# Kernel tuning notes

Hardware: AMD Instinct MI355X
Metric: run time of the kernel (lower is better)

## Reference

```python
import math
import jax, jax.numpy as jnp
import numpy as np

N_HEADS = 16


def setup_inputs() -> dict:
    key = jax.random.key(0)
    k1, k2 = jax.random.split(key)
    qkv = jax.random.normal(k1, (2, 3072, 2048), dtype=jnp.float32)
    mask = jax.random.randint(k2, (2, 1, 2048), 0, 2).astype(jnp.bool_)
    return {"qkv": qkv, "mask": mask}


def reference(qkv, mask):
    bs, width, length = qkv.shape
    ch = width // (3 * N_HEADS)
    q, k, v = jnp.split(qkv, 3, axis=1)  # each [bs, H*C, T]
    scale = 1.0 / math.sqrt(math.sqrt(ch))  # applied to both q and k
    q = (q * scale).reshape(bs * N_HEADS, ch, length)
    k = (k * scale).reshape(bs * N_HEADS, ch, length)
    # [B*H, T, T] scores
    weight = jnp.einsum('bct,bcs->bts', q, k)
    # mask: [bs, 1, T] bool, True = valid token
    inv = ~mask[:, 0, :]                      # [bs, T]
    pad = inv[:, None, :] | inv[:, :, None]   # [bs, T, T]
    pad = jnp.broadcast_to(pad[:, None], (bs, N_HEADS, length, length))
    pad = pad.reshape(bs * N_HEADS, length, length)
    weight = jnp.where(pad, jnp.finfo(weight.dtype).min, weight)
    weight = jax.nn.softmax(weight.astype(jnp.float32), axis=-1).astype(qkv.dtype)
    a = jnp.einsum('bts,bcs->bct', weight, v.reshape(bs * N_HEADS, ch, length))
    return a.reshape(bs, N_HEADS * ch, length)
```

## Files before the change

kernel.cpp:

```cpp
#include <hip/hip_runtime.h>
#include <float.h>


typedef __attribute__((ext_vector_type(8))) short bf16x8;
typedef __attribute__((ext_vector_type(4))) float f32x4;
typedef __attribute__((ext_vector_type(16))) float f32x16;

#define TSEQ 2048
#define QT_OFF 0L
#define KF_OFF 4194304L
#define VF_OFF 8388608L

#if __has_builtin(__builtin_amdgcn_exp2f)
#define EXPFN(x) __builtin_amdgcn_exp2f(x)
#define SM_SCALE (0.125f * 1.44269504088896f)
#else
#define EXPFN(x) __expf(x)
#define SM_SCALE 0.125f
#endif

__device__ inline short f2bf(float x) {
    union { float f; unsigned u; } un; un.f = x;
    unsigned r = un.u + 0x7fffu + ((un.u >> 16) & 1u);
    return (short)(r >> 16);
}

__device__ inline unsigned cvtpk(float lo, float hi) {
    unsigned r;
    asm("v_cvt_pk_bf16_f32 %0, %1, %2" : "=v"(r) : "v"(lo), "v"(hi));
    return r;
}

__device__ inline void pl32swap(unsigned &a, unsigned &b) {
    asm volatile("v_permlane32_swap_b32 %0, %1" : "+v"(a), "+v"(b));
}

__global__ __launch_bounds__(256) void prep_kernel(
    const float* __restrict__ qkv, short* __restrict__ ws)
{
    const int tid = threadIdx.x;
    const int job = blockIdx.x;
    const int tpe  = job >> 10;
    const int rest = job & 1023;
    const int bh = rest & 31, tt = rest >> 5;
    const int b = bh >> 4, h = bh & 15;

    __shared__ float Ls[64 * 65];
    const float* src = qkv + (long)b * 6291456
        + ((long)(tpe * 1024 + h * 64)) * TSEQ + tt * 64;
    #pragma unroll
    for (int ch = 0; ch < 4; ++ch) {
        int idx = tid + ch * 256;
        int c = idx >> 4, tch = idx & 15;
        float4 v = *(const float4*)(src + (long)c * TSEQ + tch * 4);
        float* L = &Ls[c * 65 + tch * 4];
        L[0] = v.x; L[1] = v.y; L[2] = v.z; L[3] = v.w;
    }
    __syncthreads();

    if (tpe == 0) {
        short* dst = ws + QT_OFF + ((long)bh * TSEQ + tt * 64) * 64;
        #pragma unroll
        for (int ch = 0; ch < 2; ++ch) {
            int idx = tid + ch * 256;
            int t = idx >> 3, cch = idx & 7;
            bf16x8 o;
            #pragma unroll
            for (int j = 0; j < 8; ++j)
                o[j] = f2bf(Ls[(cch * 8 + j) * 65 + t] * SM_SCALE);
            *(bf16x8*)(dst + (long)t * 64 + cch * 8) = o;
        }
    } else if (tpe == 1) {
        short* dst = ws + KF_OFF + (long)(bh * 32 + tt) * 4096;
        #pragma unroll
        for (int ch = 0; ch < 2; ++ch) {
            int u = tid + ch * 256;
            int f = u >> 6, lane = u & 63;
            int st = f >> 2, kk = f & 3;
            int l31 = lane & 31, H = lane >> 5;
            bf16x8 o;
            #pragma unroll
            for (int j = 0; j < 8; ++j)
                o[j] = f2bf(Ls[(kk * 16 + H * 8 + j) * 65 + st * 32 + l31]);
            *(bf16x8*)(dst + f * 512 + lane * 8) = o;
        }
    } else {
        short* dst = ws + VF_OFF + (long)(bh * 32 + tt) * 4096;
        #pragma unroll
        for (int ch = 0; ch < 2; ++ch) {
            int u = tid + ch * 256;
            int f = u >> 6, lane = u & 63;
            int ct = f >> 2, kk = f & 3;
            int l31 = lane & 31, H = lane >> 5;
            bf16x8 o;
            #pragma unroll
            for (int j = 0; j < 8; ++j)
                o[j] = f2bf(Ls[(ct * 32 + l31) * 65 + kk * 16 + H * 8 + j]);
            *(bf16x8*)(dst + f * 512 + lane * 8) = o;
        }
    }
}

__global__ __launch_bounds__(256, 4) void attn_kernel(
    const short* __restrict__ wsp, const int* __restrict__ mask,
    float* __restrict__ out)
{
    __shared__ __align__(16) char smem[17920];
    float* mbf = (float*)smem;
    float* Os  = (float*)smem;
    float* Lc  = (float*)(smem + 17408);

    const int tid  = threadIdx.x;
    const int lane = tid & 63, wid = tid >> 6;
    const int l31  = lane & 31, H = lane >> 5;
    const int wq   = wid & 1,  wss = wid >> 1;

    const int blk  = blockIdx.x;
    const int head = blk & 31;
    const int qt   = blk >> 5;
    const int b    = head >> 4, h = head & 15;
    const int t0   = qt * 64;
    const int tw   = t0 + wq * 32;

    const short* QT = wsp + QT_OFF + (long)head * 131072;
    const short* KF = wsp + KF_OFF + (long)head * 131072 + lane * 8;
    const short* VF = wsp + VF_OFF + (long)head * 131072 + lane * 8;
    const long obase = ((long)b * 1024 + h * 64) * TSEQ;

    for (int i = tid; i < TSEQ; i += 256)
        mbf[i] = (mask[b * TSEQ + i] != 0) ? 0.0f : -1e30f;
    __syncthreads();

    bf16x8 qb[4];
    #pragma unroll
    for (int kk = 0; kk < 4; ++kk)
        qb[kk] = *(const bf16x8*)(QT + (long)(tw + l31) * 64 + kk * 16 + H * 8);
    const bool qv = (mbf[tw + l31] != 0.0f);

    float l_s = 0.0f;
    f32x16 Oacc[2];
    #pragma unroll
    for (int ct = 0; ct < 2; ++ct)
        #pragma unroll
        for (int r = 0; r < 16; ++r) Oacc[ct][r] = 0.0f;

    for (int j = 0; j < 32; ++j) {
        const int ss = wss + j * 2;

        const short* kp = KF + ss * 2048;
        bf16x8 kc[4];
        #pragma unroll
        for (int kk = 0; kk < 4; ++kk)
            kc[kk] = *(const bf16x8*)(kp + kk * 512);

        const short* vp = VF + (ss >> 1) * 4096 + (ss & 1) * 1024;
        bf16x8 vf[4];
        #pragma unroll
        for (int ct = 0; ct < 2; ++ct)
            #pragma unroll
            for (int m = 0; m < 2; ++m)
                vf[ct * 2 + m] = *(const bf16x8*)(vp + ct * 2048 + m * 512);

        f32x16 Sacc;
        #pragma unroll
        for (int g = 0; g < 4; ++g) {
            f32x4 b4 = *(const f32x4*)&mbf[ss * 32 + g * 8 + H * 4];
            Sacc[4 * g + 0] = b4[0];
            Sacc[4 * g + 1] = b4[1];
            Sacc[4 * g + 2] = b4[2];
            Sacc[4 * g + 3] = b4[3];
        }

        __builtin_amdgcn_s_setprio(1);
        #pragma unroll
        for (int kk = 0; kk < 4; ++kk)
            Sacc = __builtin_amdgcn_mfma_f32_32x32x16_bf16(
                kc[kk], qb[kk], Sacc, 0, 0, 0);
        __builtin_amdgcn_s_setprio(0);

        float ls = 0.0f;
        #pragma unroll
        for (int r = 0; r < 16; ++r) {
            float e = EXPFN(Sacc[r]);
            float pv = qv ? 1.0f : e;
            ls += pv;
            Sacc[r] = pv;
        }
        l_s += ls;
        unsigned w0[4], w1[4];
        #pragma unroll
        for (int q = 0; q < 4; ++q) {
            w0[q] = cvtpk(Sacc[4 * q + 0], Sacc[4 * q + 1]);
            w1[q] = cvtpk(Sacc[4 * q + 2], Sacc[4 * q + 3]);
        }
        bf16x8 pa[2];
        #pragma unroll
        for (int kl = 0; kl < 2; ++kl) {
            unsigned a0 = w0[kl * 2], b0 = w0[kl * 2 + 1];
            unsigned a1 = w1[kl * 2], b1 = w1[kl * 2 + 1];
            pl32swap(a0, b0);
            pl32swap(a1, b1);
            union { unsigned u[4]; bf16x8 v; } cv;
            cv.u[0] = a0; cv.u[1] = a1; cv.u[2] = b0; cv.u[3] = b1;
            pa[kl] = cv.v;
        }

        __builtin_amdgcn_s_setprio(1);
        #pragma unroll
        for (int ct = 0; ct < 2; ++ct)
            #pragma unroll
            for (int m = 0; m < 2; ++m)
                Oacc[ct] = __builtin_amdgcn_mfma_f32_32x32x16_bf16(
                    pa[m], vf[ct * 2 + m], Oacc[ct], 0, 0, 0);
        __builtin_amdgcn_s_setprio(0);
    }

    __syncthreads();
    l_s += __shfl_xor(l_s, 32);
    if (lane < 32) Lc[wid * 32 + l31] = l_s;
    __syncthreads();
    const float inv = 1.0f / (l_s + Lc[(wid ^ 2) * 32 + l31]);
    float iw[16];
    #pragma unroll
    for (int r = 0; r < 16; ++r)
        iw[r] = __shfl(inv, (r & 3) + 8 * (r >> 2) + 4 * H);

    if (wss == 0) {
        #pragma unroll
        for (int ct = 0; ct < 2; ++ct) {
            const int c = ct * 32 + l31;
            #pragma unroll
            for (int g = 0; g < 4; ++g) {
                float4 o;
                o.x = Oacc[ct][4 * g + 0] * iw[4 * g + 0];
                o.y = Oacc[ct][4 * g + 1] * iw[4 * g + 1];
                o.z = Oacc[ct][4 * g + 2] * iw[4 * g + 2];
                o.w = Oacc[ct][4 * g + 3] * iw[4 * g + 3];
                *(float4*)&Os[c * 68 + wq * 32 + g * 8 + H * 4] = o;
            }
        }
    }
    __syncthreads();
    if (wss == 1) {
        #pragma unroll
        for (int ct = 0; ct < 2; ++ct) {
            const int c = ct * 32 + l31;
            #pragma unroll
            for (int g = 0; g < 4; ++g) {
                float* p = &Os[c * 68 + wq * 32 + g * 8 + H * 4];
                p[0] += Oacc[ct][4 * g + 0] * iw[4 * g + 0];
                p[1] += Oacc[ct][4 * g + 1] * iw[4 * g + 1];
                p[2] += Oacc[ct][4 * g + 2] * iw[4 * g + 2];
                p[3] += Oacc[ct][4 * g + 3] * iw[4 * g + 3];
            }
        }
    }
    __syncthreads();
    #pragma unroll
    for (int ch = 0; ch < 4; ++ch) {
        int idx = tid + ch * 256;
        int c = idx >> 4, tch = idx & 15;
        *(float4*)(out + obase + (long)c * TSEQ + t0 + tch * 4) =
            *(const float4*)&Os[c * 68 + tch * 4];
    }
}

extern "C" void kernel_launch(void* const* d_in, const int* in_sizes, int n_in,
                              void* d_out, int out_size, void* d_ws, size_t ws_size,
                              hipStream_t stream) {
    const float* qkv  = (const float*)d_in[0];
    const int*   mask = (const int*)d_in[1];
    float*       out  = (float*)d_out;
    short*       ws   = (short*)d_ws;
    prep_kernel<<<dim3(3072), dim3(256), 0, stream>>>(qkv, ws);
    attn_kernel<<<dim3(1024), dim3(256), 0, stream>>>(ws, mask, out);
}
```

Baseline: 137.2 us.

## Stage K/V tiles in LDS with double-buffered async loads, 128-query blocks

The attention kernel now has each block handle 128 queries, one 32-row slice per wave, and every wave walks all keys. Before, two waves split the key range and their partial outputs were combined through LDS. K/V tiles are loaded once per block into shared memory with global_load_lds and double-buffered across steps, so the four waves share each tile instead of each fetching from global memory. The cross-wave output reduction disappears and results are written directly to global memory. The cost is half as many blocks (512), a barrier on every key step, and less per-wave key parallelism.

```diff
diff --git a/kernel.cpp b/kernel.cpp
--- a/kernel.cpp
+++ b/kernel.cpp
@@ -18,6 +18,10 @@
 #define EXPFN(x) __expf(x)
 #define SM_SCALE 0.125f
 #endif
+
+#define GLOAD16(g, l) __builtin_amdgcn_global_load_lds( \
+    (const __attribute__((address_space(1))) void*)(g), \
+    (__attribute__((address_space(3))) void*)(l), 16, 0, 0)
 
 __device__ inline short f2bf(float x) {
     union { float f; unsigned u; } un; un.f = x;
@@ -101,41 +105,118 @@
     }
 }
 
-__global__ __launch_bounds__(256, 4) void attn_kernel(
+__device__ __forceinline__ void stageKV(
+    const char* KFb, const char* VFb, int j, char* kdst, char* vdst,
+    int wid, int lane)
+{
+    GLOAD16(KFb + (long)j * 4096 + wid * 1024 + lane * 16, kdst + wid * 1024);
+    const long voff = (long)(j >> 1) * 8192
+        + (wid >> 1) * 4096 + (j & 1) * 2048 + (wid & 1) * 1024;
+    GLOAD16(VFb + voff + lane * 16, vdst + wid * 1024);
+}
+
+__device__ __forceinline__ void computeStep(
+    int j, const short* kb, const short* vb, const float* mbf,
+    int H, int lane, bool qm,
+    const bf16x8 (&qb)[4], f32x16 (&Oacc)[2], float &l_s)
+{
+    bf16x8 kc[4];
+    #pragma unroll
+    for (int kk = 0; kk < 4; ++kk)
+        kc[kk] = *(const bf16x8*)(kb + kk * 512 + lane * 8);
+
+    f32x16 Sacc;
+    #pragma unroll
+    for (int g = 0; g < 4; ++g) {
+        f32x4 b4 = *(const f32x4*)&mbf[j * 32 + g * 8 + H * 4];
+        Sacc[4 * g + 0] = b4[0];
+        Sacc[4 * g + 1] = b4[1];
+        Sacc[4 * g + 2] = b4[2];
+        Sacc[4 * g + 3] = b4[3];
+    }
+
+    __builtin_amdgcn_s_setprio(1);
+    #pragma unroll
+    for (int kk = 0; kk < 4; ++kk)
+        Sacc = __builtin_amdgcn_mfma_f32_32x32x16_bf16(
+            kc[kk], qb[kk], Sacc, 0, 0, 0);
+    __builtin_amdgcn_s_setprio(0);
+
+    bf16x8 vf[4];
+    #pragma unroll
+    for (int w = 0; w < 4; ++w)
+        vf[w] = *(const bf16x8*)(vb + w * 512 + lane * 8);
+
+    float ls = 0.0f;
+    #pragma unroll
+    for (int r = 0; r < 16; ++r) {
+        float e = EXPFN(Sacc[r]);
+        float pv = qm ? 1.0f : e;
+        ls += pv;
+        Sacc[r] = pv;
+    }
+    l_s += ls;
+    unsigned w0[4], w1[4];
+    #pragma unroll
+    for (int q = 0; q < 4; ++q) {
+        w0[q] = cvtpk(Sacc[4 * q + 0], Sacc[4 * q + 1]);
+        w1[q] = cvtpk(Sacc[4 * q + 2], Sacc[4 * q + 3]);
+    }
+    bf16x8 pa[2];
+    #pragma unroll
+    for (int kl = 0; kl < 2; ++kl) {
+        unsigned a0 = w0[kl * 2], b0 = w0[kl * 2 + 1];
+        unsigned a1 = w1[kl * 2], b1 = w1[kl * 2 + 1];
+        pl32swap(a0, b0);
+        pl32swap(a1, b1);
+        union { unsigned u[4]; bf16x8 v; } cv;
+        cv.u[0] = a0; cv.u[1] = a1; cv.u[2] = b0; cv.u[3] = b1;
+        pa[kl] = cv.v;
+    }
+
+    __builtin_amdgcn_s_setprio(1);
+    #pragma unroll
+    for (int ct = 0; ct < 2; ++ct)
+        #pragma unroll
+        for (int m = 0; m < 2; ++m)
+            Oacc[ct] = __builtin_amdgcn_mfma_f32_32x32x16_bf16(
+                pa[m], vf[ct * 2 + m], Oacc[ct], 0, 0, 0);
+    __builtin_amdgcn_s_setprio(0);
+}
+
+__global__ __launch_bounds__(256, 2) void attn_kernel(
     const short* __restrict__ wsp, const int* __restrict__ mask,
     float* __restrict__ out)
 {
-    __shared__ __align__(16) char smem[17920];
-    float* mbf = (float*)smem;
-    float* Os  = (float*)smem;
-    float* Lc  = (float*)(smem + 17408);
+    __shared__ __align__(16) char smem[24576];
+    float* mbf = (float*)(smem + 16384);
 
     const int tid  = threadIdx.x;
     const int lane = tid & 63, wid = tid >> 6;
     const int l31  = lane & 31, H = lane >> 5;
-    const int wq   = wid & 1,  wss = wid >> 1;
 
     const int blk  = blockIdx.x;
     const int head = blk & 31;
     const int qt   = blk >> 5;
     const int b    = head >> 4, h = head & 15;
-    const int t0   = qt * 64;
-    const int tw   = t0 + wq * 32;
+    const int tw   = qt * 128 + wid * 32;
 
     const short* QT = wsp + QT_OFF + (long)head * 131072;
-    const short* KF = wsp + KF_OFF + (long)head * 131072 + lane * 8;
-    const short* VF = wsp + VF_OFF + (long)head * 131072 + lane * 8;
+    const char*  KFb = (const char*)(wsp + KF_OFF + (long)head * 131072);
+    const char*  VFb = (const char*)(wsp + VF_OFF + (long)head * 131072);
     const long obase = ((long)b * 1024 + h * 64) * TSEQ;
 
     for (int i = tid; i < TSEQ; i += 256)
         mbf[i] = (mask[b * TSEQ + i] != 0) ? 0.0f : -1e30f;
+
+    stageKV(KFb, VFb, 0, smem, smem + 4096, wid, lane);
     __syncthreads();
 
     bf16x8 qb[4];
     #pragma unroll
     for (int kk = 0; kk < 4; ++kk)
         qb[kk] = *(const bf16x8*)(QT + (long)(tw + l31) * 64 + kk * 16 + H * 8);
-    const bool qv = (mbf[tw + l31] != 0.0f);
+    const bool qm = (mbf[tw + l31] != 0.0f);
 
     float l_s = 0.0f;
     f32x16 Oacc[2];
@@ -144,124 +225,44 @@
         #pragma unroll
         for (int r = 0; r < 16; ++r) Oacc[ct][r] = 0.0f;
 
-    for (int j = 0; j < 32; ++j) {
-        const int ss = wss + j * 2;
-
-        const short* kp = KF + ss * 2048;
-        bf16x8 kc[4];
-        #pragma unroll
-        for (int kk = 0; kk < 4; ++kk)
-            kc[kk] = *(const bf16x8*)(kp + kk * 512);
-
-        const short* vp = VF + (ss >> 1) * 4096 + (ss & 1) * 1024;
-        bf16x8 vf[4];
-        #pragma unroll
-        for (int ct = 0; ct < 2; ++ct)
-            #pragma unroll
-            for (int m = 0; m < 2; ++m)
-                vf[ct * 2 + m] = *(const bf16x8*)(vp + ct * 2048 + m * 512);
-
-        f32x16 Sacc;
-        #pragma unroll
-        for (int g = 0; g < 4; ++g) {
-            f32x4 b4 = *(const f32x4*)&mbf[ss * 32 + g * 8 + H * 4];
-            Sacc[4 * g + 0] = b4[0];
-            Sacc[4 * g + 1] = b4[1];
-            Sacc[4 * g + 2] = b4[2];
-            Sacc[4 * g + 3] = b4[3];
-        }
-
-        __builtin_amdgcn_s_setprio(1);
-        #pragma unroll
-        for (int kk = 0; kk < 4; ++kk)
-            Sacc = __builtin_amdgcn_mfma_f32_32x32x16_bf16(
-                kc[kk], qb[kk], Sacc, 0, 0, 0);
-        __builtin_amdgcn_s_setprio(0);
-
-        float ls = 0.0f;
-        #pragma unroll
-        for (int r = 0; r < 16; ++r) {
-            float e = EXPFN(Sacc[r]);
-            float pv = qv ? 1.0f : e;
-            ls += pv;
-            Sacc[r] = pv;
-        }
-        l_s += ls;
-        unsigned w0[4], w1[4];
-        #pragma unroll
-        for (int q = 0; q < 4; ++q) {
-            w0[q] = cvtpk(Sacc[4 * q + 0], Sacc[4 * q + 1]);
-            w1[q] = cvtpk(Sacc[4 * q + 2], Sacc[4 * q + 3]);
-        }
-        bf16x8 pa[2];
-        #pragma unroll
-        for (int kl = 0; kl < 2; ++kl) {
-            unsigned a0 = w0[kl * 2], b0 = w0[kl * 2 + 1];
-            unsigned a1 = w1[kl * 2], b1 = w1[kl * 2 + 1];
-            pl32swap(a0, b0);
-            pl32swap(a1, b1);
-            union { unsigned u[4]; bf16x8 v; } cv;
-            cv.u[0] = a0; cv.u[1] = a1; cv.u[2] = b0; cv.u[3] = b1;
-            pa[kl] = cv.v;
-        }
-
-        __builtin_amdgcn_s_setprio(1);
-        #pragma unroll
-        for (int ct = 0; ct < 2; ++ct)
-            #pragma unroll
-            for (int m = 0; m < 2; ++m)
-                Oacc[ct] = __builtin_amdgcn_mfma_f32_32x32x16_bf16(
-                    pa[m], vf[ct * 2 + m], Oacc[ct], 0, 0, 0);
-        __builtin_amdgcn_s_setprio(0);
-    }
-
+    const short* kb0 = (const short*)smem;
+    const short* vb0 = (const short*)(smem + 4096);
+    const short* kb1 = (const short*)(smem + 8192);
+    const short* vb1 = (const short*)(smem + 12288);
+
+    for (int jj = 0; jj < 31; ++jj) {
+        const int jA = 2 * jj, jB = 2 * jj + 1;
+        stageKV(KFb, VFb, jB, smem + 8192, smem + 12288, wid, lane);
+        computeStep(jA, kb0, vb0, mbf, H, lane, qm, qb, Oacc, l_s);
+        __syncthreads();
+        stageKV(KFb, VFb, jB + 1, smem, smem + 4096, wid, lane);
+        computeStep(jB, kb1, vb1, mbf, H, lane, qm, qb, Oacc, l_s);
+        __syncthreads();
+    }
+    stageKV(KFb, VFb, 63, smem + 8192, smem + 12288, wid, lane);
+    computeStep(62, kb0, vb0, mbf, H, lane, qm, qb, Oacc, l_s);
     __syncthreads();
+    computeStep(63, kb1, vb1, mbf, H, lane, qm, qb, Oacc, l_s);
+
     l_s += __shfl_xor(l_s, 32);
-    if (lane < 32) Lc[wid * 32 + l31] = l_s;
-    __syncthreads();
-    const float inv = 1.0f / (l_s + Lc[(wid ^ 2) * 32 + l31]);
+    const float inv = 1.0f / l_s;
     float iw[16];
     #pragma unroll
     for (int r = 0; r < 16; ++r)
         iw[r] = __shfl(inv, (r & 3) + 8 * (r >> 2) + 4 * H);
 
-    if (wss == 0) {
-        #pragma unroll
-        for (int ct = 0; ct < 2; ++ct) {
-            const int c = ct * 32 + l31;
-            #pragma unroll
-            for (int g = 0; g < 4; ++g) {
-                float4 o;
-                o.x = Oacc[ct][4 * g + 0] * iw[4 * g + 0];
-                o.y = Oacc[ct][4 * g + 1] * iw[4 * g + 1];
-                o.z = Oacc[ct][4 * g + 2] * iw[4 * g + 2];
-                o.w = Oacc[ct][4 * g + 3] * iw[4 * g + 3];
-                *(float4*)&Os[c * 68 + wq * 32 + g * 8 + H * 4] = o;
-            }
-        }
-    }
-    __syncthreads();
-    if (wss == 1) {
-        #pragma unroll
-        for (int ct = 0; ct < 2; ++ct) {
-            const int c = ct * 32 + l31;
-            #pragma unroll
-            for (int g = 0; g < 4; ++g) {
-                float* p = &Os[c * 68 + wq * 32 + g * 8 + H * 4];
-                p[0] += Oacc[ct][4 * g + 0] * iw[4 * g + 0];
-                p[1] += Oacc[ct][4 * g + 1] * iw[4 * g + 1];
-                p[2] += Oacc[ct][4 * g + 2] * iw[4 * g + 2];
-                p[3] += Oacc[ct][4 * g + 3] * iw[4 * g + 3];
-            }
-        }
-    }
-    __syncthreads();
-    #pragma unroll
-    for (int ch = 0; ch < 4; ++ch) {
-        int idx = tid + ch * 256;
-        int c = idx >> 4, tch = idx & 15;
-        *(float4*)(out + obase + (long)c * TSEQ + t0 + tch * 4) =
-            *(const float4*)&Os[c * 68 + tch * 4];
+    #pragma unroll
+    for (int ct = 0; ct < 2; ++ct) {
+        const int c = ct * 32 + l31;
+        #pragma unroll
+        for (int g = 0; g < 4; ++g) {
+            float4 o;
+            o.x = Oacc[ct][4 * g + 0] * iw[4 * g + 0];
+            o.y = Oacc[ct][4 * g + 1] * iw[4 * g + 1];
+            o.z = Oacc[ct][4 * g + 2] * iw[4 * g + 2];
+            o.w = Oacc[ct][4 * g + 3] * iw[4 * g + 3];
+            *(float4*)(out + obase + (long)c * TSEQ + tw + g * 8 + H * 4) = o;
+        }
     }
 }
 
@@ -273,5 +274,5 @@
     float*       out  = (float*)d_out;
     short*       ws   = (short*)d_ws;
     prep_kernel<<<dim3(3072), dim3(256), 0, stream>>>(qkv, ws);
-    attn_kernel<<<dim3(1024), dim3(256), 0, stream>>>(ws, mask, out);
-}
+    attn_kernel<<<dim3(512), dim3(256), 0, stream>>>(ws, mask, out);
+}
```

Result: faster. 130.2 us (-5.1%).
